# Kernel optimization log

Measured on AMD Instinct MI355X. Metric: run time of the kernel, lower is better.

Reference implementation:

```python
import math
import jax, jax.numpy as jnp
import numpy as np

IN_CH = 256
BIG, SMALL = 15, 3
GHOST_RATIO = 0.23
NK = math.ceil(BIG / SMALL)           # 5
PAD = SMALL // 2                       # 1
MID = BIG // 2                         # 7
REAL_PAD = [MID - i * SMALL - PAD for i in range(NK)]  # [6,3,0,-3,-6]

# Replicate the torch module's deterministic ghost/rep channel split
np.random.seed(123)
_ghostN = int(IN_CH * GHOST_RATIO)     # 58
REPN = IN_CH - _ghostN                 # 198
_ghost = np.sort(np.random.choice(IN_CH, _ghostN, replace=False))
_rep = np.array(sorted(set(range(IN_CH)) - set(_ghost.tolist())), dtype=np.int64)

B, L = 32, 4096
EPS = 1e-5


def _bn(x, g, b):
    # training-mode BatchNorm1d over (B, L) per channel
    m = jnp.mean(x, (0, 2), keepdims=True)
    v = jnp.var(x, (0, 2), keepdims=True)
    return (x - m) * jax.lax.rsqrt(v + EPS) * g[None, :, None] + b[None, :, None]


def _shift(x, p):
    # zero-filled shift along L: out[t] = x[t - p]
    Lx = x.shape[-1]
    if p > 0:
        return jnp.pad(x, ((0, 0), (0, 0), (p, 0)))[..., :Lx]
    if p < 0:
        return jnp.pad(x, ((0, 0), (0, 0), (0, -p)))[..., -Lx:]
    return x


def setup_inputs() -> dict:
    key = jax.random.key(0)
    ks = jax.random.split(key, 3)
    inputs = jax.random.normal(ks[0], (B, IN_CH, L), dtype=jnp.float32)
    lora_w1 = jax.random.normal(ks[1], (REPN * NK, 1, SMALL), dtype=jnp.float32) * 0.1
    lora_w2 = jax.random.normal(ks[2], (REPN * NK, 1, SMALL), dtype=jnp.float32) * 0.1
    ones = jnp.ones((REPN,), jnp.float32)
    zeros = jnp.zeros((REPN,), jnp.float32)
    return {"inputs": inputs, "lora_w1": lora_w1, "lora_w2": lora_w2,
            "gamma1": ones, "beta1": zeros, "gamma2": ones, "beta2": zeros,
            "gamma3": ones, "beta3": zeros}


def reference(inputs, lora_w1, lora_w2, gamma1, beta1, gamma2, beta2, gamma3, beta3):
    rep_in = inputs[:, _rep, :]        # [B, repN, L]
    ghost_in = inputs[:, _ghost, :]    # [B, ghostN, L]
    # sum of N_path depthwise convs == one conv with summed weights
    w = lora_w1 + lora_w2              # [repN*nk, 1, small]
    out = jax.lax.conv_general_dilated(
        rep_in, w, window_strides=(1,), padding=[(PAD, PAD)],
        dimension_numbers=("NCH", "OIH", "NCH"), feature_group_count=REPN)
    b, _, l = out.shape
    o = out.reshape(b, REPN, NK, l)    # torch grouped conv: group-major channel order
    # shift-add decomposition: reconstruct big-kernel responses from nk small-conv slices
    x1 = sum(_shift(o[:, :, i, :], REAL_PAD[i]) for i in range(NK))
    x2 = sum(_shift(o[:, :, i, :], -REAL_PAD[i]) for i in range(NK))
    x3 = o[:, :, NK // 2, :]           # zero-shift (small-kernel) slice
    x1 = _bn(x1, gamma1, beta1)
    x2 = _bn(x2, gamma2, beta2)
    x3 = _bn(x3, gamma3, beta3)
    x = x1 + x2 + x3 + rep_in
    return jnp.concatenate([x, ghost_in], axis=1)  # [B, C, L]
```

## Files before the change

kernel.cpp:

```cpp
#include <hip/hip_runtime.h>

#define LEN 4096
#define BATCH 32
#define CH 256
#define REPN 198
#define GHOSTN 58
#define NROW (REPN * BATCH)
#define NGHOST (GHOSTN * BATCH)
#define P1REPBLK 3168
#define P2REPBLK 3168

typedef float f32x4 __attribute__((ext_vector_type(4)));

struct MTState { unsigned mt[624]; int mti; };
struct Tab { int rep[REPN]; int ghost[GHOSTN]; };

static constexpr unsigned mt_next(MTState& s) {
    if (s.mti >= 624) {
        for (int k = 0; k < 624; ++k) {
            unsigned y = (s.mt[k] & 0x80000000u) | (s.mt[(k + 1) % 624] & 0x7fffffffu);
            s.mt[k] = s.mt[(k + 397) % 624] ^ (y >> 1) ^ ((y & 1u) ? 0x9908b0dfu : 0u);
        }
        s.mti = 0;
    }
    unsigned y = s.mt[s.mti++];
    y ^= y >> 11;
    y ^= (y << 7) & 0x9d2c5680u;
    y ^= (y << 15) & 0xefc60000u;
    y ^= y >> 18;
    return y;
}

static constexpr Tab make_tab() {
    MTState s{};
    s.mt[0] = 123u;
    for (int i = 1; i < 624; ++i)
        s.mt[i] = 1812433253u * (s.mt[i - 1] ^ (s.mt[i - 1] >> 30)) + (unsigned)i;
    s.mti = 624;
    int perm[256] = {};
    for (int i = 0; i < 256; ++i) perm[i] = i;
    for (int i = 255; i > 0; --i) {
        unsigned mask = (unsigned)i;
        mask |= mask >> 1; mask |= mask >> 2; mask |= mask >> 4;
        mask |= mask >> 8; mask |= mask >> 16;
        unsigned j = 0;
        do { j = mt_next(s) & mask; } while (j > (unsigned)i);
        int t = perm[i]; perm[i] = perm[j]; perm[j] = t;
    }
    bool g[256] = {};
    for (int k = 0; k < GHOSTN; ++k) g[perm[k]] = true;
    Tab t{};
    int rc = 0, gc = 0;
    for (int c = 0; c < 256; ++c) {
        if (g[c]) t.ghost[gc++] = c;
        else      t.rep[rc++] = c;
    }
    return t;
}

__constant__ Tab d_tab = make_tab();

#define C1F(D) wb[(D) / 3][(D) % 3]
#define C2F(D) wb[4 - (D) / 3][(D) % 3]

__global__ __launch_bounds__(256) void pass1_kernel(const float* __restrict__ x,
                                                    const float* __restrict__ w1,
                                                    const float* __restrict__ w2,
                                                    float* __restrict__ stats_ws,
                                                    float* __restrict__ out) {
    const int blk = blockIdx.x;
    if (blk >= P1REPBLK) {
        const int g = (blk - P1REPBLK) % GHOSTN;
        const int b = (blk - P1REPBLK) / GHOSTN;
        const int ch = d_tab.ghost[g];
        const f32x4* src = (const f32x4*)(x + ((size_t)b * CH + ch) * LEN);
        f32x4* dst = (f32x4*)(out + ((size_t)b * CH + REPN + g) * LEN);
#pragma unroll
        for (int k = 0; k < 4; ++k) {
            f32x4 t = __builtin_nontemporal_load(&src[threadIdx.x + 256 * k]);
            dst[threadIdx.x + 256 * k] = t;
        }
        return;
    }

    __shared__ float comb[4][22];
    const int widx = threadIdx.x >> 6;
    const int lane = threadIdx.x & 63;
    const int rowid = (blk << 1) | (widx >> 1);
    const int half = widx & 1;
    const int r = rowid % REPN;
    const int b = rowid / REPN;
    const float* row = x + ((size_t)b * CH + d_tab.rep[r]) * LEN;

    float A[15];
#pragma unroll
    for (int dl = 0; dl < 15; ++dl) A[dl] = 0.f;
    float SX = 0.f;
    float B0[8], B1[8], B2[8], B3[8], B4[8], B5[8];
    const int base = (half << 11) + (lane << 5);

#define LOAD8(DST, OFF)                                                           \
    {                                                                             \
        if ((OFF) < LEN) {                                                        \
            const f32x4* q4_ = (const f32x4*)(row + (OFF));                       \
            f32x4 u0_ = q4_[0], u1_ = q4_[1];                                     \
            DST[0] = u0_.x; DST[1] = u0_.y; DST[2] = u0_.z; DST[3] = u0_.w;       \
            DST[4] = u1_.x; DST[5] = u1_.y; DST[6] = u1_.z; DST[7] = u1_.w;       \
        } else {                                                                  \
            _Pragma("unroll")                                                     \
            for (int t = 0; t < 8; ++t) DST[t] = 0.f;                             \
        }                                                                         \
    }

#define ACC8(P, Q, R)                                                             \
    {                                                                             \
        _Pragma("unroll")                                                         \
        for (int j = 0; j < 8; ++j) {                                             \
            const float xj_ = P[j];                                               \
            SX += xj_;                                                            \
            _Pragma("unroll")                                                     \
            for (int dl = 0; dl < 15; ++dl) {                                     \
                const int t_ = j + dl;                                            \
                const float xd_ = (t_ < 8) ? P[t_]                                \
                                 : (t_ < 16) ? Q[t_ - 8] : R[t_ - 16];            \
                A[dl] = fmaf(xj_, xd_, A[dl]);                                    \
            }                                                                     \
        }                                                                         \
    }

    LOAD8(B0, base);
    LOAD8(B1, base + 8);
    LOAD8(B2, base + 16);
    LOAD8(B3, base + 24);
    LOAD8(B4, base + 32);
    LOAD8(B5, base + 40);
    ACC8(B0, B1, B2);
    ACC8(B1, B2, B3);
    ACC8(B2, B3, B4);
    ACC8(B3, B4, B5);
#undef LOAD8
#undef ACC8

    float wb[5][3];
    {
        const float* p1 = w1 + r * 15;
        const float* p2 = w2 + r * 15;
#pragma unroll
        for (int i = 0; i < 5; ++i)
#pragma unroll
            for (int t = 0; t < 3; ++t) wb[i][t] = p1[i * 3 + t] + p2[i * 3 + t];
    }

    float d1 = 0.f, d1q = 0.f, d2 = 0.f, d2q = 0.f, d3 = 0.f, d3q = 0.f;
    if (half == 0 && lane < 26) {
        const int l = (lane <= 12) ? (lane - 7) : (4090 + (lane - 13));
        float u1 = 0.f, u2 = 0.f, u3 = 0.f, g1 = 0.f, g2 = 0.f;
#pragma unroll
        for (int d = 0; d < 15; ++d) {
            const int p = l + d - 7;
            const float xd = ((unsigned)p < (unsigned)LEN) ? row[p] : 0.f;
            const float a1 = C1F(d) * xd;
            const float a2 = C2F(d) * xd;
            u1 += a1; u2 += a2;
            if (d >= 6 && d <= 8) u3 += a1;
            const bool gate = ((unsigned)(l - 6 + 3 * (d / 3)) < (unsigned)LEN);
            g1 += gate ? a1 : 0.f;
            g2 += gate ? a2 : 0.f;
        }
        if ((unsigned)l < (unsigned)LEN) {
            d1 = g1 - u1;  d1q = fmaf(g1, g1, -u1 * u1);
            d2 = g2 - u2;  d2q = fmaf(g2, g2, -u2 * u2);
        } else {
            d1 = -u1;  d1q = -u1 * u1;
            d2 = -u2;  d2q = -u2 * u2;
            d3 = -u3;  d3q = -u3 * u3;
        }
    }

#pragma unroll
    for (int off = 32; off > 0; off >>= 1) {
#pragma unroll
        for (int dl = 0; dl < 15; ++dl) A[dl] += __shfl_down(A[dl], off);
        SX += __shfl_down(SX, off);
        d1 += __shfl_down(d1, off);   d1q += __shfl_down(d1q, off);
        d2 += __shfl_down(d2, off);   d2q += __shfl_down(d2q, off);
        d3 += __shfl_down(d3, off);   d3q += __shfl_down(d3q, off);
    }

    if (lane == 0) {
#pragma unroll
        for (int dl = 0; dl < 15; ++dl) comb[widx][dl] = A[dl];
        comb[widx][15] = SX;
        comb[widx][16] = d1;  comb[widx][17] = d1q;
        comb[widx][18] = d2;  comb[widx][19] = d2q;
        comb[widx][20] = d3;  comb[widx][21] = d3q;
    }
    __syncthreads();

    if (half == 0 && lane == 0) {
        float Af[15];
#pragma unroll
        for (int dl = 0; dl < 15; ++dl) Af[dl] = comb[widx][dl] + comb[widx + 1][dl];
        const float SXf = comb[widx][15] + comb[widx + 1][15];
        const float e1  = comb[widx][16] + comb[widx + 1][16];
        const float e1q = comb[widx][17] + comb[widx + 1][17];
        const float e2  = comb[widx][18] + comb[widx + 1][18];
        const float e2q = comb[widx][19] + comb[widx + 1][19];
        const float e3  = comb[widx][20] + comb[widx + 1][20];
        const float e3q = comb[widx][21] + comb[widx + 1][21];

        float sq1 = 0.f, sq2 = 0.f;
#pragma unroll
        for (int dl = 0; dl < 15; ++dl) {
            float r1 = 0.f, r2 = 0.f;
#pragma unroll
            for (int d = 0; d + dl < 15; ++d) {
                r1 = fmaf(C1F(d), C1F(d + dl), r1);
                r2 = fmaf(C2F(d), C2F(d + dl), r2);
            }
            const float wA = (dl ? 2.f : 1.f) * Af[dl];
            sq1 = fmaf(r1, wA, sq1);
            sq2 = fmaf(r2, wA, sq2);
        }
        const float c30 = wb[2][0], c31 = wb[2][1], c32 = wb[2][2];
        float sq3 = (c30 * c30 + c31 * c31 + c32 * c32) * Af[0]
                  + 2.f * (c30 * c31 + c31 * c32) * Af[1]
                  + 2.f * (c30 * c32) * Af[2];
        float cs = 0.f;
#pragma unroll
        for (int i = 0; i < 5; ++i)
#pragma unroll
            for (int t = 0; t < 3; ++t) cs += wb[i][t];
        const float c3s = c30 + c31 + c32;

        stats_ws[(0 * REPN + r) * BATCH + b] = fmaf(cs, SXf, e1);
        stats_ws[(1 * REPN + r) * BATCH + b] = sq1 + e1q;
        stats_ws[(2 * REPN + r) * BATCH + b] = fmaf(cs, SXf, e2);
        stats_ws[(3 * REPN + r) * BATCH + b] = sq2 + e2q;
        stats_ws[(4 * REPN + r) * BATCH + b] = fmaf(c3s, SXf, e3);
        stats_ws[(5 * REPN + r) * BATCH + b] = sq3 + e3q;
    }
}

__device__ __forceinline__ void load_fast(const float* __restrict__ row, int e, float* v) {
    const f32x4* q4 = (const f32x4*)(row + e - 8);
#pragma unroll
    for (int t = 0; t < 5; ++t) {
        f32x4 u = q4[t];
        v[4 * t] = u.x; v[4 * t + 1] = u.y; v[4 * t + 2] = u.z; v[4 * t + 3] = u.w;
    }
}

__device__ __forceinline__ void load_slow(const float* __restrict__ row, int e, float* v) {
#pragma unroll
    for (int d = 0; d < 20; ++d) {
        int fi = e - 8 + d;
        v[d] = ((unsigned)fi < (unsigned)LEN) ? row[fi] : 0.f;
    }
}

__global__ __launch_bounds__(256) void pass2_kernel(const float* __restrict__ x,
                                                    const float* __restrict__ w1,
                                                    const float* __restrict__ w2,
                                                    const float* __restrict__ stats_ws,
                                                    const float* __restrict__ g1, const float* __restrict__ b1,
                                                    const float* __restrict__ g2, const float* __restrict__ b2,
                                                    const float* __restrict__ g3, const float* __restrict__ b3,
                                                    float* __restrict__ out) {
    const int wv = (blockIdx.x << 2) | (threadIdx.x >> 6);
    const int lane = threadIdx.x & 63;
    const int rowid = wv >> 1;
    const int half = wv & 1;
    const int r = rowid % REPN;
    const int b = rowid / REPN;
    const int ch = d_tab.rep[r];
    const float* row = x + ((size_t)b * CH + ch) * LEN;

    float p[6];
    const int bb = lane & 31;
#pragma unroll
    for (int q = 0; q < 6; ++q) p[q] = stats_ws[(q * REPN + r) * BATCH + bb];
#pragma unroll
    for (int m = 1; m < 32; m <<= 1)
#pragma unroll
        for (int q = 0; q < 6; ++q) p[q] += __shfl_xor(p[q], m);

    const double invN = 1.0 / (double)(BATCH * LEN);
    float sc[3], sh[3];
    {
        const float gr[3] = {g1[r], g2[r], g3[r]};
        const float br[3] = {b1[r], b2[r], b3[r]};
#pragma unroll
        for (int q = 0; q < 3; ++q) {
            double mean = (double)p[2 * q] * invN;
            double var = (double)p[2 * q + 1] * invN - mean * mean;
            double inv = 1.0 / sqrt(var + 1e-5);
            double scale = (double)gr[q] * inv;
            sc[q] = (float)scale;
            sh[q] = (float)((double)br[q] - mean * scale);
        }
    }
    const float base = sh[0] + sh[1] + sh[2];

    float wb[5][3];
    const float* p1 = w1 + r * 15;
    const float* p2 = w2 + r * 15;
#pragma unroll
    for (int i = 0; i < 5; ++i)
#pragma unroll
        for (int t = 0; t < 3; ++t) wb[i][t] = p1[i * 3 + t] + p2[i * 3 + t];

    float c[15];
#pragma unroll
    for (int k = 0; k < 5; ++k)
#pragma unroll
        for (int t = 0; t < 3; ++t)
            c[3 * k + t] = fmaf(sc[0], wb[k][t], sc[1] * wb[4 - k][t]);
#pragma unroll
    for (int t = 0; t < 3; ++t) c[6 + t] = fmaf(sc[2], wb[2][t], c[6 + t]);

    float* orow = out + ((size_t)b * CH + r) * LEN;
    float vA[20], vB[20];

#define INTERIOR_QUAD(E, V)                                                       \
    {                                                                             \
        float o[4];                                                               \
        _Pragma("unroll")                                                         \
        for (int j = 0; j < 4; ++j) {                                             \
            float acc = base + V[j + 8];                                          \
            _Pragma("unroll")                                                     \
            for (int d = 0; d < 15; ++d) acc = fmaf(c[d], V[j + 1 + d], acc);     \
            o[j] = acc;                                                           \
        }                                                                         \
        f32x4 t = {o[0], o[1], o[2], o[3]};                                       \
        *(f32x4*)(orow + (E)) = t;                                                \
    }

#define EDGE_QUAD(E, V)                                                           \
    {                                                                             \
        float o[4];                                                               \
        _Pragma("unroll")                                                         \
        for (int j = 0; j < 4; ++j) {                                             \
            const int l = (E) + j;                                                \
            float x1 = 0.f, x2 = 0.f, x3 = 0.f;                                   \
            _Pragma("unroll")                                                     \
            for (int i = 0; i < 5; ++i) {                                         \
                float a1 = fmaf(wb[i][0], V[j + 1 + 3 * i],                       \
                           fmaf(wb[i][1], V[j + 2 + 3 * i],                       \
                                wb[i][2] * V[j + 3 + 3 * i]));                    \
                float a2 = fmaf(wb[i][0], V[j + 13 - 3 * i],                      \
                           fmaf(wb[i][1], V[j + 14 - 3 * i],                      \
                                wb[i][2] * V[j + 15 - 3 * i]));                   \
                if (i == 2) x3 = a1;                                              \
                a1 = ((unsigned)(l - 6 + 3 * i) < (unsigned)LEN) ? a1 : 0.f;      \
                a2 = ((unsigned)(l + 6 - 3 * i) < (unsigned)LEN) ? a2 : 0.f;      \
                x1 += a1; x2 += a2;                                               \
            }                                                                     \
            o[j] = fmaf(sc[0], x1, fmaf(sc[1], x2, fmaf(sc[2], x3, base + V[j + 8]))); \
        }                                                                         \
        f32x4 t = {o[0], o[1], o[2], o[3]};                                       \
        *(f32x4*)(orow + (E)) = t;                                                \
    }

    if (half == 0) {
        {
            const int e = 4 * lane;
            if (lane < 2) { load_slow(row, e, vA); EDGE_QUAD(e, vA); }
            else          { load_fast(row, e, vA); INTERIOR_QUAD(e, vA); }
        }
        load_fast(row, 4 * lane + 256, vA);
#pragma unroll
        for (int kk = 0; kk < 3; ++kk) {
            const int k = 1 + 2 * kk;
            const int eA = 4 * lane + 256 * k;
            const int eB = eA + 256;
            load_fast(row, eB, vB);
            INTERIOR_QUAD(eA, vA);
            load_fast(row, eB + 256, vA);
            INTERIOR_QUAD(eB, vB);
        }
        INTERIOR_QUAD(4 * lane + 256 * 7, vA);
    } else {
        load_fast(row, 4 * lane + 256 * 8, vA);
#pragma unroll
        for (int kk = 0; kk < 3; ++kk) {
            const int k = 8 + 2 * kk;
            const int eA = 4 * lane + 256 * k;
            const int eB = eA + 256;
            load_fast(row, eB, vB);
            INTERIOR_QUAD(eA, vA);
            load_fast(row, eB + 256, vA);
            INTERIOR_QUAD(eB, vB);
        }
        INTERIOR_QUAD(4 * lane + 256 * 14, vA);
        {
            const int e = 4 * lane + 3840;
            if (lane >= 62) { load_slow(row, e, vA); EDGE_QUAD(e, vA); }
            else            { load_fast(row, e, vA); INTERIOR_QUAD(e, vA); }
        }
    }
#undef INTERIOR_QUAD
#undef EDGE_QUAD
}

extern "C" void kernel_launch(void* const* d_in, const int* in_sizes, int n_in,
                              void* d_out, int out_size, void* d_ws, size_t ws_size,
                              hipStream_t stream) {
    const float* x  = (const float*)d_in[0];
    const float* w1 = (const float*)d_in[1];
    const float* w2 = (const float*)d_in[2];
    const float* g1 = (const float*)d_in[3];
    const float* b1 = (const float*)d_in[4];
    const float* g2 = (const float*)d_in[5];
    const float* b2 = (const float*)d_in[6];
    const float* g3 = (const float*)d_in[7];
    const float* b3 = (const float*)d_in[8];
    float* out = (float*)d_out;
    float* stats_ws = (float*)d_ws;

    pass1_kernel<<<P1REPBLK + NGHOST, 256, 0, stream>>>(x, w1, w2, stats_ws, out);
    pass2_kernel<<<P2REPBLK, 256, 0, stream>>>(x, w1, w2, stats_ws,
                                               g1, b1, g2, b2, g3, b3, out);
}
```

Baseline: 78.53 us.

## Split each row across four waves instead of two in both passes

Both kernels now give one row to a whole block of four waves, each wave covering a quarter of the row, instead of two half-row waves per block. Pass1 cuts its per-thread register buffers from six to four 8-float chunks, and the edge-correction work moves to waves 0 and 3. The final reduction now sums four partials. This doubles the grid size and raises parallelism and latency hiding, at the cost of more blocks and more per-row reduction and statistics overhead.

```diff
diff --git a/kernel.cpp b/kernel.cpp
--- a/kernel.cpp
+++ b/kernel.cpp
@@ -7,8 +7,6 @@
 #define GHOSTN 58
 #define NROW (REPN * BATCH)
 #define NGHOST (GHOSTN * BATCH)
-#define P1REPBLK 3168
-#define P2REPBLK 3168
 
 typedef float f32x4 __attribute__((ext_vector_type(4)));
 
@@ -69,9 +67,9 @@
                                                     float* __restrict__ stats_ws,
                                                     float* __restrict__ out) {
     const int blk = blockIdx.x;
-    if (blk >= P1REPBLK) {
-        const int g = (blk - P1REPBLK) % GHOSTN;
-        const int b = (blk - P1REPBLK) / GHOSTN;
+    if (blk >= NROW) {
+        const int g = (blk - NROW) % GHOSTN;
+        const int b = (blk - NROW) / GHOSTN;
         const int ch = d_tab.ghost[g];
         const f32x4* src = (const f32x4*)(x + ((size_t)b * CH + ch) * LEN);
         f32x4* dst = (f32x4*)(out + ((size_t)b * CH + REPN + g) * LEN);
@@ -86,18 +84,16 @@
     __shared__ float comb[4][22];
     const int widx = threadIdx.x >> 6;
     const int lane = threadIdx.x & 63;
-    const int rowid = (blk << 1) | (widx >> 1);
-    const int half = widx & 1;
-    const int r = rowid % REPN;
-    const int b = rowid / REPN;
+    const int r = blk % REPN;
+    const int b = blk / REPN;
     const float* row = x + ((size_t)b * CH + d_tab.rep[r]) * LEN;
 
     float A[15];
 #pragma unroll
     for (int dl = 0; dl < 15; ++dl) A[dl] = 0.f;
     float SX = 0.f;
-    float B0[8], B1[8], B2[8], B3[8], B4[8], B5[8];
-    const int base = (half << 11) + (lane << 5);
+    float B0[8], B1[8], B2[8], B3[8];
+    const int base = (widx << 10) + (lane << 4);
 
 #define LOAD8(DST, OFF)                                                           \
     {                                                                             \
@@ -132,12 +128,8 @@
     LOAD8(B1, base + 8);
     LOAD8(B2, base + 16);
     LOAD8(B3, base + 24);
-    LOAD8(B4, base + 32);
-    LOAD8(B5, base + 40);
     ACC8(B0, B1, B2);
     ACC8(B1, B2, B3);
-    ACC8(B2, B3, B4);
-    ACC8(B3, B4, B5);
 #undef LOAD8
 #undef ACC8
 
@@ -152,8 +144,8 @@
     }
 
     float d1 = 0.f, d1q = 0.f, d2 = 0.f, d2q = 0.f, d3 = 0.f, d3q = 0.f;
-    if (half == 0 && lane < 26) {
-        const int l = (lane <= 12) ? (lane - 7) : (4090 + (lane - 13));
+    if ((widx == 0 || widx == 3) && lane < 13) {
+        const int l = (widx == 0) ? (lane - 7) : (4090 + lane);
         float u1 = 0.f, u2 = 0.f, u3 = 0.f, g1 = 0.f, g2 = 0.f;
 #pragma unroll
         for (int d = 0; d < 15; ++d) {
@@ -197,17 +189,18 @@
     }
     __syncthreads();
 
-    if (half == 0 && lane == 0) {
+    if (widx == 0 && lane == 0) {
         float Af[15];
 #pragma unroll
-        for (int dl = 0; dl < 15; ++dl) Af[dl] = comb[widx][dl] + comb[widx + 1][dl];
-        const float SXf = comb[widx][15] + comb[widx + 1][15];
-        const float e1  = comb[widx][16] + comb[widx + 1][16];
-        const float e1q = comb[widx][17] + comb[widx + 1][17];
-        const float e2  = comb[widx][18] + comb[widx + 1][18];
-        const float e2q = comb[widx][19] + comb[widx + 1][19];
-        const float e3  = comb[widx][20] + comb[widx + 1][20];
-        const float e3q = comb[widx][21] + comb[widx + 1][21];
+        for (int dl = 0; dl < 15; ++dl)
+            Af[dl] = (comb[0][dl] + comb[1][dl]) + (comb[2][dl] + comb[3][dl]);
+        const float SXf = (comb[0][15] + comb[1][15]) + (comb[2][15] + comb[3][15]);
+        const float e1  = comb[0][16] + comb[3][16];
+        const float e1q = comb[0][17] + comb[3][17];
+        const float e2  = comb[0][18] + comb[3][18];
+        const float e2q = comb[0][19] + comb[3][19];
+        const float e3  = comb[0][20] + comb[3][20];
+        const float e3q = comb[0][21] + comb[3][21];
 
         float sq1 = 0.f, sq2 = 0.f;
 #pragma unroll
@@ -269,8 +262,8 @@
                                                     float* __restrict__ out) {
     const int wv = (blockIdx.x << 2) | (threadIdx.x >> 6);
     const int lane = threadIdx.x & 63;
-    const int rowid = wv >> 1;
-    const int half = wv & 1;
+    const int rowid = wv >> 2;
+    const int q = wv & 3;
     const int r = rowid % REPN;
     const int b = rowid / REPN;
     const int ch = d_tab.rep[r];
@@ -279,11 +272,11 @@
     float p[6];
     const int bb = lane & 31;
 #pragma unroll
-    for (int q = 0; q < 6; ++q) p[q] = stats_ws[(q * REPN + r) * BATCH + bb];
+    for (int qq = 0; qq < 6; ++qq) p[qq] = stats_ws[(qq * REPN + r) * BATCH + bb];
 #pragma unroll
     for (int m = 1; m < 32; m <<= 1)
 #pragma unroll
-        for (int q = 0; q < 6; ++q) p[q] += __shfl_xor(p[q], m);
+        for (int qq = 0; qq < 6; ++qq) p[qq] += __shfl_xor(p[qq], m);
 
     const double invN = 1.0 / (double)(BATCH * LEN);
     float sc[3], sh[3];
@@ -291,13 +284,13 @@
         const float gr[3] = {g1[r], g2[r], g3[r]};
         const float br[3] = {b1[r], b2[r], b3[r]};
 #pragma unroll
-        for (int q = 0; q < 3; ++q) {
-            double mean = (double)p[2 * q] * invN;
-            double var = (double)p[2 * q + 1] * invN - mean * mean;
+        for (int qq = 0; qq < 3; ++qq) {
+            double mean = (double)p[2 * qq] * invN;
+            double var = (double)p[2 * qq + 1] * invN - mean * mean;
             double inv = 1.0 / sqrt(var + 1e-5);
-            double scale = (double)gr[q] * inv;
-            sc[q] = (float)scale;
-            sh[q] = (float)((double)br[q] - mean * scale);
+            double scale = (double)gr[qq] * inv;
+            sc[qq] = (float)scale;
+            sh[qq] = (float)((double)br[qq] - mean * scale);
         }
     }
     const float base = sh[0] + sh[1] + sh[2];
@@ -362,42 +355,41 @@
         *(f32x4*)(orow + (E)) = t;                                                \
     }
 
-    if (half == 0) {
+    if (q == 0) {
         {
             const int e = 4 * lane;
             if (lane < 2) { load_slow(row, e, vA); EDGE_QUAD(e, vA); }
             else          { load_fast(row, e, vA); INTERIOR_QUAD(e, vA); }
         }
         load_fast(row, 4 * lane + 256, vA);
-#pragma unroll
-        for (int kk = 0; kk < 3; ++kk) {
-            const int k = 1 + 2 * kk;
-            const int eA = 4 * lane + 256 * k;
-            const int eB = eA + 256;
-            load_fast(row, eB, vB);
-            INTERIOR_QUAD(eA, vA);
-            load_fast(row, eB + 256, vA);
-            INTERIOR_QUAD(eB, vB);
-        }
-        INTERIOR_QUAD(4 * lane + 256 * 7, vA);
-    } else {
-        load_fast(row, 4 * lane + 256 * 8, vA);
-#pragma unroll
-        for (int kk = 0; kk < 3; ++kk) {
-            const int k = 8 + 2 * kk;
-            const int eA = 4 * lane + 256 * k;
-            const int eB = eA + 256;
-            load_fast(row, eB, vB);
-            INTERIOR_QUAD(eA, vA);
-            load_fast(row, eB + 256, vA);
-            INTERIOR_QUAD(eB, vB);
-        }
+        load_fast(row, 4 * lane + 512, vB);
+        INTERIOR_QUAD(4 * lane + 256, vA);
+        load_fast(row, 4 * lane + 768, vA);
+        INTERIOR_QUAD(4 * lane + 512, vB);
+        INTERIOR_QUAD(4 * lane + 768, vA);
+    } else if (q == 3) {
+        load_fast(row, 4 * lane + 256 * 12, vA);
+        load_fast(row, 4 * lane + 256 * 13, vB);
+        INTERIOR_QUAD(4 * lane + 256 * 12, vA);
+        load_fast(row, 4 * lane + 256 * 14, vA);
+        INTERIOR_QUAD(4 * lane + 256 * 13, vB);
         INTERIOR_QUAD(4 * lane + 256 * 14, vA);
         {
             const int e = 4 * lane + 3840;
             if (lane >= 62) { load_slow(row, e, vA); EDGE_QUAD(e, vA); }
             else            { load_fast(row, e, vA); INTERIOR_QUAD(e, vA); }
         }
+    } else {
+        const int kb = q << 2;
+        const int e0 = 4 * lane + 256 * kb;
+        load_fast(row, e0, vA);
+        load_fast(row, e0 + 256, vB);
+        INTERIOR_QUAD(e0, vA);
+        load_fast(row, e0 + 512, vA);
+        INTERIOR_QUAD(e0 + 256, vB);
+        load_fast(row, e0 + 768, vB);
+        INTERIOR_QUAD(e0 + 512, vA);
+        INTERIOR_QUAD(e0 + 768, vB);
     }
 #undef INTERIOR_QUAD
 #undef EDGE_QUAD
@@ -418,7 +410,7 @@
     float* out = (float*)d_out;
     float* stats_ws = (float*)d_ws;
 
-    pass1_kernel<<<P1REPBLK + NGHOST, 256, 0, stream>>>(x, w1, w2, stats_ws, out);
-    pass2_kernel<<<P2REPBLK, 256, 0, stream>>>(x, w1, w2, stats_ws,
-                                               g1, b1, g2, b2, g3, b3, out);
-}
+    pass1_kernel<<<NROW + NGHOST, 256, 0, stream>>>(x, w1, w2, stats_ws, out);
+    pass2_kernel<<<NROW, 256, 0, stream>>>(x, w1, w2, stats_ws,
+                                           g1, b1, g2, b2, g3, b3, out);
+}
```

New measurement: 92.99 us. 18.4% more time.

## Split pass2 rows across four waves and prefetch data before stats reduction

Applied to the files above, without the earlier changes.

Pass2 now gives each block a single row, with four waves each covering a quarter of it, where before each wave handled half a row. Each wave issues its first input loads before the BN statistics reduction. Only wave 0 reduces the statistics and broadcasts scale and shift through shared memory after a barrier. This hides the stats reduction and double-precision math behind the loads and removes redundant per-wave reductions, at the cost of a block barrier and a shorter per-wave pipeline.

```diff
diff --git a/kernel.cpp b/kernel.cpp
--- a/kernel.cpp
+++ b/kernel.cpp
@@ -8,7 +8,6 @@
 #define NROW (REPN * BATCH)
 #define NGHOST (GHOSTN * BATCH)
 #define P1REPBLK 3168
-#define P2REPBLK 3168
 
 typedef float f32x4 __attribute__((ext_vector_type(4)));
 
@@ -267,60 +266,78 @@
                                                     const float* __restrict__ g2, const float* __restrict__ b2,
                                                     const float* __restrict__ g3, const float* __restrict__ b3,
                                                     float* __restrict__ out) {
-    const int wv = (blockIdx.x << 2) | (threadIdx.x >> 6);
+    __shared__ float cb[4];
     const int lane = threadIdx.x & 63;
-    const int rowid = wv >> 1;
-    const int half = wv & 1;
+    const int q = threadIdx.x >> 6;
+    const int rowid = blockIdx.x;
     const int r = rowid % REPN;
     const int b = rowid / REPN;
     const int ch = d_tab.rep[r];
     const float* row = x + ((size_t)b * CH + ch) * LEN;
-
-    float p[6];
-    const int bb = lane & 31;
-#pragma unroll
-    for (int q = 0; q < 6; ++q) p[q] = stats_ws[(q * REPN + r) * BATCH + bb];
-#pragma unroll
-    for (int m = 1; m < 32; m <<= 1)
-#pragma unroll
-        for (int q = 0; q < 6; ++q) p[q] += __shfl_xor(p[q], m);
-
-    const double invN = 1.0 / (double)(BATCH * LEN);
-    float sc[3], sh[3];
-    {
+    float* orow = out + ((size_t)b * CH + r) * LEN;
+
+    float vA[20], vB[20];
+    if (q == 0) {
+        const int e = 4 * lane;
+        if (lane < 2) load_slow(row, e, vA); else load_fast(row, e, vA);
+        load_fast(row, 4 * lane + 256, vB);
+    } else if (q == 3) {
+        load_fast(row, 4 * lane + 3072, vA);
+        load_fast(row, 4 * lane + 3328, vB);
+    } else {
+        const int e0 = 4 * lane + 1024 * q;
+        load_fast(row, e0, vA);
+        load_fast(row, e0 + 256, vB);
+    }
+
+    if (q == 0) {
+        float p[6];
+        const int bb = lane & 31;
+#pragma unroll
+        for (int qq = 0; qq < 6; ++qq) p[qq] = stats_ws[(qq * REPN + r) * BATCH + bb];
+#pragma unroll
+        for (int m = 1; m < 32; m <<= 1)
+#pragma unroll
+            for (int qq = 0; qq < 6; ++qq) p[qq] += __shfl_xor(p[qq], m);
+
+        const double invN = 1.0 / (double)(BATCH * LEN);
         const float gr[3] = {g1[r], g2[r], g3[r]};
         const float br[3] = {b1[r], b2[r], b3[r]};
-#pragma unroll
-        for (int q = 0; q < 3; ++q) {
-            double mean = (double)p[2 * q] * invN;
-            double var = (double)p[2 * q + 1] * invN - mean * mean;
+        float scl[3], shf[3];
+#pragma unroll
+        for (int qq = 0; qq < 3; ++qq) {
+            double mean = (double)p[2 * qq] * invN;
+            double var = (double)p[2 * qq + 1] * invN - mean * mean;
             double inv = 1.0 / sqrt(var + 1e-5);
-            double scale = (double)gr[q] * inv;
-            sc[q] = (float)scale;
-            sh[q] = (float)((double)br[q] - mean * scale);
-        }
-    }
-    const float base = sh[0] + sh[1] + sh[2];
+            double scale = (double)gr[qq] * inv;
+            scl[qq] = (float)scale;
+            shf[qq] = (float)((double)br[qq] - mean * scale);
+        }
+        if (lane == 0) {
+            cb[0] = scl[0]; cb[1] = scl[1]; cb[2] = scl[2];
+            cb[3] = shf[0] + shf[1] + shf[2];
+        }
+    }
+    __syncthreads();
+    const float sc0 = cb[0], sc1 = cb[1], sc2 = cb[2], base = cb[3];
 
     float wb[5][3];
-    const float* p1 = w1 + r * 15;
-    const float* p2 = w2 + r * 15;
-#pragma unroll
-    for (int i = 0; i < 5; ++i)
-#pragma unroll
-        for (int t = 0; t < 3; ++t) wb[i][t] = p1[i * 3 + t] + p2[i * 3 + t];
-
+    {
+        const float* p1 = w1 + r * 15;
+        const float* p2 = w2 + r * 15;
+#pragma unroll
+        for (int i = 0; i < 5; ++i)
+#pragma unroll
+            for (int t = 0; t < 3; ++t) wb[i][t] = p1[i * 3 + t] + p2[i * 3 + t];
+    }
     float c[15];
 #pragma unroll
     for (int k = 0; k < 5; ++k)
 #pragma unroll
         for (int t = 0; t < 3; ++t)
-            c[3 * k + t] = fmaf(sc[0], wb[k][t], sc[1] * wb[4 - k][t]);
-#pragma unroll
-    for (int t = 0; t < 3; ++t) c[6 + t] = fmaf(sc[2], wb[2][t], c[6 + t]);
-
-    float* orow = out + ((size_t)b * CH + r) * LEN;
-    float vA[20], vB[20];
+            c[3 * k + t] = fmaf(sc0, wb[k][t], sc1 * wb[4 - k][t]);
+#pragma unroll
+    for (int t = 0; t < 3; ++t) c[6 + t] = fmaf(sc2, wb[2][t], c[6 + t]);
 
 #define INTERIOR_QUAD(E, V)                                                       \
     {                                                                             \
@@ -356,48 +373,40 @@
                 a2 = ((unsigned)(l + 6 - 3 * i) < (unsigned)LEN) ? a2 : 0.f;      \
                 x1 += a1; x2 += a2;                                               \
             }                                                                     \
-            o[j] = fmaf(sc[0], x1, fmaf(sc[1], x2, fmaf(sc[2], x3, base + V[j + 8]))); \
+            o[j] = fmaf(sc0, x1, fmaf(sc1, x2, fmaf(sc2, x3, base + V[j + 8])));  \
         }                                                                         \
         f32x4 t = {o[0], o[1], o[2], o[3]};                                       \
         *(f32x4*)(orow + (E)) = t;                                                \
     }
 
-    if (half == 0) {
+    if (q == 0) {
         {
             const int e = 4 * lane;
-            if (lane < 2) { load_slow(row, e, vA); EDGE_QUAD(e, vA); }
-            else          { load_fast(row, e, vA); INTERIOR_QUAD(e, vA); }
-        }
-        load_fast(row, 4 * lane + 256, vA);
-#pragma unroll
-        for (int kk = 0; kk < 3; ++kk) {
-            const int k = 1 + 2 * kk;
-            const int eA = 4 * lane + 256 * k;
-            const int eB = eA + 256;
-            load_fast(row, eB, vB);
-            INTERIOR_QUAD(eA, vA);
-            load_fast(row, eB + 256, vA);
-            INTERIOR_QUAD(eB, vB);
-        }
-        INTERIOR_QUAD(4 * lane + 256 * 7, vA);
-    } else {
-        load_fast(row, 4 * lane + 256 * 8, vA);
-#pragma unroll
-        for (int kk = 0; kk < 3; ++kk) {
-            const int k = 8 + 2 * kk;
-            const int eA = 4 * lane + 256 * k;
-            const int eB = eA + 256;
-            load_fast(row, eB, vB);
-            INTERIOR_QUAD(eA, vA);
-            load_fast(row, eB + 256, vA);
-            INTERIOR_QUAD(eB, vB);
-        }
-        INTERIOR_QUAD(4 * lane + 256 * 14, vA);
+            if (lane < 2) { EDGE_QUAD(e, vA); } else { INTERIOR_QUAD(e, vA); }
+        }
+        load_fast(row, 4 * lane + 512, vA);
+        INTERIOR_QUAD(4 * lane + 256, vB);
+        load_fast(row, 4 * lane + 768, vB);
+        INTERIOR_QUAD(4 * lane + 512, vA);
+        INTERIOR_QUAD(4 * lane + 768, vB);
+    } else if (q == 3) {
+        INTERIOR_QUAD(4 * lane + 3072, vA);
+        load_fast(row, 4 * lane + 3584, vA);
+        INTERIOR_QUAD(4 * lane + 3328, vB);
         {
             const int e = 4 * lane + 3840;
-            if (lane >= 62) { load_slow(row, e, vA); EDGE_QUAD(e, vA); }
-            else            { load_fast(row, e, vA); INTERIOR_QUAD(e, vA); }
-        }
+            if (lane >= 62) load_slow(row, e, vB); else load_fast(row, e, vB);
+            INTERIOR_QUAD(4 * lane + 3584, vA);
+            if (lane >= 62) { EDGE_QUAD(e, vB); } else { INTERIOR_QUAD(e, vB); }
+        }
+    } else {
+        const int e0 = 4 * lane + 1024 * q;
+        INTERIOR_QUAD(e0, vA);
+        load_fast(row, e0 + 512, vA);
+        INTERIOR_QUAD(e0 + 256, vB);
+        load_fast(row, e0 + 768, vB);
+        INTERIOR_QUAD(e0 + 512, vA);
+        INTERIOR_QUAD(e0 + 768, vB);
     }
 #undef INTERIOR_QUAD
 #undef EDGE_QUAD
@@ -419,6 +428,6 @@
     float* stats_ws = (float*)d_ws;
 
     pass1_kernel<<<P1REPBLK + NGHOST, 256, 0, stream>>>(x, w1, w2, stats_ws, out);
-    pass2_kernel<<<P2REPBLK, 256, 0, stream>>>(x, w1, w2, stats_ws,
-                                               g1, b1, g2, b2, g3, b3, out);
-}
+    pass2_kernel<<<NROW, 256, 0, stream>>>(x, w1, w2, stats_ws,
+                                           g1, b1, g2, b2, g3, b3, out);
+}
```

After: 85.67 us. +9.1%, slower.
